# Kernel tuning notes

Hardware: AMD Instinct MI355X
Metric: run time of the kernel (lower is better)

The kernel has to match this reference:

```python
import jax, jax.numpy as jnp
import numpy as np

B, N, D_NODE, D_GRAPH = 512, 512, 128, 128
EPS = 1e-12  # torch F.normalize eps


def setup_inputs() -> dict:
    key = jax.random.key(0)
    k_h, k_ns, k_wf, k_bf, k_wg, k_bg = jax.random.split(key, 6)
    s = 1.0 / np.sqrt(D_NODE)
    return {
        "h": jax.random.normal(k_h, (B, N, D_NODE), dtype=jnp.float32),
        "ns": jax.random.randint(k_ns, (B,), 1, N + 1, dtype=jnp.int64),
        "W_f": jax.random.uniform(k_wf, (D_GRAPH, D_NODE), jnp.float32, -s, s),
        "b_f": jax.random.uniform(k_bf, (D_GRAPH,), jnp.float32, -s, s),
        "W_g": jax.random.uniform(k_wg, (1, D_NODE), jnp.float32, -s, s),
        "b_g": jax.random.uniform(k_bg, (1,), jnp.float32, -s, s),
    }


def reference(h, ns, W_f, b_f, W_g, b_g):
    # h: [B, N, D_node]; ns: [B] valid node counts per graph
    h_vG = jnp.einsum("bnd,ed->bne", h, W_f) + b_f          # [B, N, D_graph]
    g_vG = jax.nn.sigmoid(jnp.einsum("bnd,od->bno", h, W_g) + b_g)  # [B, N, 1]
    mask = (jnp.arange(N) < ns[:, None])[:, :, None]         # [B, N, 1]
    h_G = jnp.sum(h_vG * g_vG * mask, axis=1)                # [B, D_graph]
    norm = jnp.linalg.norm(h_G, axis=-1, keepdims=True)
    return h_G / jnp.maximum(norm, EPS)
```

## Files before the change

### kernel.cpp

```cpp
#include <hip/hip_runtime.h>
#include <math.h>

#define BB 512
#define NN 512
#define DD 128

__global__ __launch_bounds__(1024) void k_graph(
    const float* __restrict__ h,
    const int*   __restrict__ ns,
    const float* __restrict__ W_g,
    const float* __restrict__ b_g,
    const float* __restrict__ W_f,
    const float* __restrict__ b_f,
    float*       __restrict__ out)
{
    const int b    = blockIdx.x;
    const int tid  = threadIdx.x;
    const int grp  = tid >> 5;
    const int lane = tid & 31;

    const int end = ns[b];

    __shared__ float lds_s[32 * 128];
    __shared__ float lds_t[32];
    __shared__ float red[2];

    const float4 wg = ((const float4*)W_g)[lane];
    const float  bg = b_g[0];
    const float4* hb = (const float4*)(h + (size_t)b * NN * DD);

    float4 acc  = make_float4(0.f, 0.f, 0.f, 0.f);
    float  tacc = 0.f;

    for (int n = grp; n < end; n += 128) {
        const int  n1 = n + 32, n2 = n + 64, n3 = n + 96;
        const int  r1 = n1 < end ? n1 : end - 1;
        const int  r2 = n2 < end ? n2 : end - 1;
        const int  r3 = n3 < end ? n3 : end - 1;
        const float m1 = n1 < end ? 1.f : 0.f;
        const float m2 = n2 < end ? 1.f : 0.f;
        const float m3 = n3 < end ? 1.f : 0.f;

        const float4 v0 = hb[(size_t)n  * 32 + lane];
        const float4 v1 = hb[(size_t)r1 * 32 + lane];
        const float4 v2 = hb[(size_t)r2 * 32 + lane];
        const float4 v3 = hb[(size_t)r3 * 32 + lane];

        float d0 = v0.x * wg.x + v0.y * wg.y + v0.z * wg.z + v0.w * wg.w;
        float d1 = v1.x * wg.x + v1.y * wg.y + v1.z * wg.z + v1.w * wg.w;
        float d2 = v2.x * wg.x + v2.y * wg.y + v2.z * wg.z + v2.w * wg.w;
        float d3 = v3.x * wg.x + v3.y * wg.y + v3.z * wg.z + v3.w * wg.w;
        #pragma unroll
        for (int m = 1; m <= 16; m <<= 1) {
            d0 += __shfl_xor(d0, m);
            d1 += __shfl_xor(d1, m);
            d2 += __shfl_xor(d2, m);
            d3 += __shfl_xor(d3, m);
        }
        const float g0 =      1.f / (1.f + expf(-(d0 + bg)));
        const float g1 = m1 * (1.f / (1.f + expf(-(d1 + bg))));
        const float g2 = m2 * (1.f / (1.f + expf(-(d2 + bg))));
        const float g3 = m3 * (1.f / (1.f + expf(-(d3 + bg))));

        acc.x += g0 * v0.x + g1 * v1.x + g2 * v2.x + g3 * v3.x;
        acc.y += g0 * v0.y + g1 * v1.y + g2 * v2.y + g3 * v3.y;
        acc.z += g0 * v0.z + g1 * v1.z + g2 * v2.z + g3 * v3.z;
        acc.w += g0 * v0.w + g1 * v1.w + g2 * v2.w + g3 * v3.w;
        tacc  += g0 + g1 + g2 + g3;
    }

    ((float4*)lds_s)[grp * 32 + lane] = acc;
    if (lane == 0) lds_t[grp] = tacc;
    __syncthreads();

    float s = 0.f, t = 0.f;
    if (tid < 128) {
        #pragma unroll
        for (int g2 = 0; g2 < 32; ++g2) s += lds_s[g2 * 128 + tid];
        #pragma unroll
        for (int g2 = 0; g2 < 32; ++g2) t += lds_t[g2];
    }
    __syncthreads();
    if (tid < 128) lds_s[tid] = s;
    __syncthreads();

    float hg = 0.f;
    if (tid < 128) {
        hg = t * b_f[tid];
        const float4* wrow = (const float4*)(W_f + (size_t)tid * DD);
        const float4* sv   = (const float4*)lds_s;
        #pragma unroll 8
        for (int k = 0; k < 32; ++k) {
            const float4 w  = wrow[k];
            const float4 sk = sv[k];
            hg += w.x * sk.x + w.y * sk.y + w.z * sk.z + w.w * sk.w;
        }
        float sq = hg * hg;
        sq += __shfl_xor(sq, 1);
        sq += __shfl_xor(sq, 2);
        sq += __shfl_xor(sq, 4);
        sq += __shfl_xor(sq, 8);
        sq += __shfl_xor(sq, 16);
        sq += __shfl_xor(sq, 32);
        if ((tid & 63) == 0) red[tid >> 6] = sq;
    }
    __syncthreads();
    if (tid < 128) {
        const float norm = sqrtf(red[0] + red[1]);
        out[(size_t)b * DD + tid] = hg / fmaxf(norm, 1e-12f);
    }
}

extern "C" void kernel_launch(void* const* d_in, const int* in_sizes, int n_in,
                              void* d_out, int out_size, void* d_ws, size_t ws_size,
                              hipStream_t stream) {
    const float* h   = (const float*)d_in[0];
    const int*   ns  = (const int*)  d_in[1];
    const float* W_f = (const float*)d_in[2];
    const float* b_f = (const float*)d_in[3];
    const float* W_g = (const float*)d_in[4];
    const float* b_g = (const float*)d_in[5];
    float* out = (float*)d_out;

    k_graph<<<BB, 1024, 0, stream>>>(h, ns, W_g, b_g, W_f, b_f, out);
}
```

Baseline: 25.32 us.

## Remap rows to 8-lane subgroups with 512-thread blocks and hardware exp/rcp

Switches from 32-lane groups handling four rows per iteration to 64-lane wavefronts where each 8-lane subgroup loads a full row as four float4s. The gate dot product now needs only three shuffle steps per row, and the sigmoid uses raw v_exp_f32/v_rcp_f32 instead of expf and a division. Cross-subgroup reduction moves to shuffles after the loop, and the LDS reduction shrinks from 32 to 8 partials. Blocks drop to 512 threads, so each thread carries more accumulators and memory-level parallelism per thread changes. The hardware exp and reciprocal are slightly less precise than the library calls.

Result: faster. 21.68 us (-14.4%).

```diff
diff --git a/kernel.cpp b/kernel.cpp
--- a/kernel.cpp
+++ b/kernel.cpp
@@ -5,7 +5,7 @@
 #define NN 512
 #define DD 128
 
-__global__ __launch_bounds__(1024) void k_graph(
+__global__ __launch_bounds__(512) void k_graph(
     const float* __restrict__ h,
     const int*   __restrict__ ns,
     const float* __restrict__ W_g,
@@ -16,69 +16,93 @@
 {
     const int b    = blockIdx.x;
     const int tid  = threadIdx.x;
-    const int grp  = tid >> 5;
-    const int lane = tid & 31;
+    const int wv   = tid >> 6;
+    const int lane = tid & 63;
+    const int sub  = lane & 7;
+    const int rowg = lane >> 3;
 
     const int end = ns[b];
 
-    __shared__ float lds_s[32 * 128];
-    __shared__ float lds_t[32];
+    __shared__ float lds_s[8 * 128];
+    __shared__ float lds_t[8];
     __shared__ float red[2];
 
-    const float4 wg = ((const float4*)W_g)[lane];
-    const float  bg = b_g[0];
+    const float4 wg0 = ((const float4*)W_g)[ 0 + sub];
+    const float4 wg1 = ((const float4*)W_g)[ 8 + sub];
+    const float4 wg2 = ((const float4*)W_g)[16 + sub];
+    const float4 wg3 = ((const float4*)W_g)[24 + sub];
+    const float  bg  = b_g[0];
+
     const float4* hb = (const float4*)(h + (size_t)b * NN * DD);
 
-    float4 acc  = make_float4(0.f, 0.f, 0.f, 0.f);
+    float4 a0 = make_float4(0.f,0.f,0.f,0.f);
+    float4 a1 = make_float4(0.f,0.f,0.f,0.f);
+    float4 a2 = make_float4(0.f,0.f,0.f,0.f);
+    float4 a3 = make_float4(0.f,0.f,0.f,0.f);
     float  tacc = 0.f;
 
-    for (int n = grp; n < end; n += 128) {
-        const int  n1 = n + 32, n2 = n + 64, n3 = n + 96;
-        const int  r1 = n1 < end ? n1 : end - 1;
-        const int  r2 = n2 < end ? n2 : end - 1;
-        const int  r3 = n3 < end ? n3 : end - 1;
-        const float m1 = n1 < end ? 1.f : 0.f;
-        const float m2 = n2 < end ? 1.f : 0.f;
-        const float m3 = n3 < end ? 1.f : 0.f;
+    for (int n0 = wv * 8; n0 < end; n0 += 64) {
+        int r = n0 + rowg;
+        const float valid = (r < end) ? 1.f : 0.f;
+        r = (r < end) ? r : (end - 1);
+        const float4* rp = hb + (size_t)r * 32 + sub;
+        const float4 v0 = rp[ 0];
+        const float4 v1 = rp[ 8];
+        const float4 v2 = rp[16];
+        const float4 v3 = rp[24];
 
-        const float4 v0 = hb[(size_t)n  * 32 + lane];
-        const float4 v1 = hb[(size_t)r1 * 32 + lane];
-        const float4 v2 = hb[(size_t)r2 * 32 + lane];
-        const float4 v3 = hb[(size_t)r3 * 32 + lane];
+        float d = v0.x*wg0.x + v0.y*wg0.y + v0.z*wg0.z + v0.w*wg0.w
+                + v1.x*wg1.x + v1.y*wg1.y + v1.z*wg1.z + v1.w*wg1.w
+                + v2.x*wg2.x + v2.y*wg2.y + v2.z*wg2.z + v2.w*wg2.w
+                + v3.x*wg3.x + v3.y*wg3.y + v3.z*wg3.z + v3.w*wg3.w;
+        d += __shfl_xor(d, 1);
+        d += __shfl_xor(d, 2);
+        d += __shfl_xor(d, 4);
 
-        float d0 = v0.x * wg.x + v0.y * wg.y + v0.z * wg.z + v0.w * wg.w;
-        float d1 = v1.x * wg.x + v1.y * wg.y + v1.z * wg.z + v1.w * wg.w;
-        float d2 = v2.x * wg.x + v2.y * wg.y + v2.z * wg.z + v2.w * wg.w;
-        float d3 = v3.x * wg.x + v3.y * wg.y + v3.z * wg.z + v3.w * wg.w;
-        #pragma unroll
-        for (int m = 1; m <= 16; m <<= 1) {
-            d0 += __shfl_xor(d0, m);
-            d1 += __shfl_xor(d1, m);
-            d2 += __shfl_xor(d2, m);
-            d3 += __shfl_xor(d3, m);
-        }
-        const float g0 =      1.f / (1.f + expf(-(d0 + bg)));
-        const float g1 = m1 * (1.f / (1.f + expf(-(d1 + bg))));
-        const float g2 = m2 * (1.f / (1.f + expf(-(d2 + bg))));
-        const float g3 = m3 * (1.f / (1.f + expf(-(d3 + bg))));
+        const float texp = (d + bg) * -1.44269504f;
+        float e;
+        asm("v_exp_f32 %0, %1" : "=v"(e) : "v"(texp));
+        const float ep1 = e + 1.f;
+        float gr;
+        asm("v_rcp_f32 %0, %1" : "=v"(gr) : "v"(ep1));
+        const float g = valid * gr;
 
-        acc.x += g0 * v0.x + g1 * v1.x + g2 * v2.x + g3 * v3.x;
-        acc.y += g0 * v0.y + g1 * v1.y + g2 * v2.y + g3 * v3.y;
-        acc.z += g0 * v0.z + g1 * v1.z + g2 * v2.z + g3 * v3.z;
-        acc.w += g0 * v0.w + g1 * v1.w + g2 * v2.w + g3 * v3.w;
-        tacc  += g0 + g1 + g2 + g3;
+        a0.x += g*v0.x; a0.y += g*v0.y; a0.z += g*v0.z; a0.w += g*v0.w;
+        a1.x += g*v1.x; a1.y += g*v1.y; a1.z += g*v1.z; a1.w += g*v1.w;
+        a2.x += g*v2.x; a2.y += g*v2.y; a2.z += g*v2.z; a2.w += g*v2.w;
+        a3.x += g*v3.x; a3.y += g*v3.y; a3.z += g*v3.z; a3.w += g*v3.w;
+        tacc += g;
     }
 
-    ((float4*)lds_s)[grp * 32 + lane] = acc;
-    if (lane == 0) lds_t[grp] = tacc;
+    #pragma unroll
+    for (int m = 8; m <= 32; m <<= 1) {
+        a0.x += __shfl_xor(a0.x, m); a0.y += __shfl_xor(a0.y, m);
+        a0.z += __shfl_xor(a0.z, m); a0.w += __shfl_xor(a0.w, m);
+        a1.x += __shfl_xor(a1.x, m); a1.y += __shfl_xor(a1.y, m);
+        a1.z += __shfl_xor(a1.z, m); a1.w += __shfl_xor(a1.w, m);
+        a2.x += __shfl_xor(a2.x, m); a2.y += __shfl_xor(a2.y, m);
+        a2.z += __shfl_xor(a2.z, m); a2.w += __shfl_xor(a2.w, m);
+        a3.x += __shfl_xor(a3.x, m); a3.y += __shfl_xor(a3.y, m);
+        a3.z += __shfl_xor(a3.z, m); a3.w += __shfl_xor(a3.w, m);
+        tacc += __shfl_xor(tacc, m);
+    }
+
+    if (rowg == 0) {
+        float4* dst = (float4*)lds_s + wv * 32;
+        dst[ 0 + sub] = a0;
+        dst[ 8 + sub] = a1;
+        dst[16 + sub] = a2;
+        dst[24 + sub] = a3;
+        if (sub == 0) lds_t[wv] = tacc;
+    }
     __syncthreads();
 
     float s = 0.f, t = 0.f;
     if (tid < 128) {
         #pragma unroll
-        for (int g2 = 0; g2 < 32; ++g2) s += lds_s[g2 * 128 + tid];
+        for (int g2 = 0; g2 < 8; ++g2) s += lds_s[g2 * 128 + tid];
         #pragma unroll
-        for (int g2 = 0; g2 < 32; ++g2) t += lds_t[g2];
+        for (int g2 = 0; g2 < 8; ++g2) t += lds_t[g2];
     }
     __syncthreads();
     if (tid < 128) lds_s[tid] = s;
@@ -122,5 +146,5 @@
     const float* b_g = (const float*)d_in[5];
     float* out = (float*)d_out;
 
-    k_graph<<<BB, 1024, 0, stream>>>(h, ns, W_g, b_g, W_f, b_f, out);
+    k_graph<<<BB, 512, 0, stream>>>(h, ns, W_g, b_g, W_f, b_f, out);
 }
```
